# Performance work log

Measured on AMD Instinct MI355X. Metric: run time of the kernel, lower is better.

The kernel has to match this reference:

```python
import jax, jax.numpy as jnp
import numpy as np

B, N, CIN = 8, 4096, 64
S, K, C = 1024, 32, 128      # npoint, k, out_channels
J, DEPTH, H = 5, 2, 4
BETA, EPS = 0.05, 1e-5


def _fps(xyz, npoint):
    # farthest point sampling, deterministic start at index 0
    Bb, Nn = xyz.shape[0], xyz.shape[1]
    bidx = jnp.arange(Bb)

    def step(carry, _):
        dist, far = carry
        cen = xyz[bidx, far][:, None, :]              # [B,1,3]
        d = jnp.sum((xyz - cen) ** 2, -1)             # [B,N]
        dist = jnp.minimum(dist, d)
        nxt = jnp.argmax(dist, axis=1).astype(jnp.int32)
        return (dist, nxt), far

    init = (jnp.full((Bb, Nn), 1e10, xyz.dtype), jnp.zeros((Bb,), jnp.int32))
    _, idxs = jax.lax.scan(step, init, None, length=npoint)
    return idxs.T                                      # [B,npoint]


def _ln(x, g, b):
    mu = jnp.mean(x, -1, keepdims=True)
    v = jnp.mean((x - mu) ** 2, -1, keepdims=True)
    return (x - mu) * jax.lax.rsqrt(v + EPS) * g + b


def _forward(xyz, points, w1, g1, b1, w2, g2, b2, w3, g3, b3,
             ws, wb, alpha, wqkv, wo, ln1g, ln1b, ln2g, ln2b):
    gather = jax.vmap(lambda a, i: a[i])
    fps_idx = _fps(xyz, S)
    new_xyz = gather(xyz, fps_idx)                     # [B,S,3]
    # kNN: squared distances from centroids to all points
    d2 = (jnp.sum(new_xyz ** 2, -1)[:, :, None] + jnp.sum(xyz ** 2, -1)[:, None, :]
          - 2.0 * jnp.einsum('bsd,bnd->bsn', new_xyz, xyz))   # [B,S,N]
    idx = jax.lax.top_k(-d2, K)[1]                     # [B,S,K]
    flat = idx.reshape(B, S * K)
    gxyz = gather(xyz, flat).reshape(B, S, K, 3)
    gnorm = gxyz - new_xyz[:, :, None, :]              # relative coords
    gpts = gather(points, flat).reshape(B, S, K, CIN)
    h = jnp.concatenate([gnorm, gpts], -1)             # [B,S,K,67]
    # pointwise shared MLP (1x1 conv + BN(batch stats) + ReLU)
    for w, g, b in ((w1, g1, b1), (w2, g2, b2), (w3, g3, b3)):
        h = jnp.einsum('bskc,oc->bsko', h, w)
        m = jnp.mean(h, (0, 1, 2))
        v = jnp.var(h, (0, 1, 2))
        h = jax.nn.relu((h - m) * jax.lax.rsqrt(v + EPS) * g + b)
    P = B * S
    pf = h.reshape(P, K, C)
    px = gnorm.reshape(P, K, 3)
    # per-patch graph: Gaussian affinity, sigma = mean pairwise distance
    dd = jnp.sum((px[:, :, None] - px[:, None, :]) ** 2, -1)   # [P,K,K]
    sigma = jnp.mean(jnp.sqrt(dd + 1e-12), (1, 2))[:, None, None]
    A = jnp.exp(-dd / (2.0 * sigma ** 2 + 1e-12))
    dinv = jax.lax.rsqrt(jnp.sum(A, -1) + 1e-12)
    I = jnp.eye(K, dtype=pf.dtype)
    L = I - dinv[:, :, None] * A * dinv[:, None, :]
    # heat-kernel wavelets psi_j = exp(-s_j L), 4th-order Taylor
    psis = []
    for j in range(J):
        M = (-BETA * (2.0 ** j)) * L
        T = I + M
        acc = M
        for m in range(2, 5):
            acc = jnp.einsum('pkl,plm->pkm', acc, M) / m
            T = T + acc
        psis.append(T)
    hcur = pf
    for d in range(DEPTH):
        mix = jnp.zeros_like(hcur)
        for j in range(J):
            mix = mix + alpha[d, j] * jnp.einsum('pkl,plc,cd->pkd', psis[j], hcur, ws[d, j])
        hcur = _ln(hcur + jax.nn.relu(mix + wb[d]), ln1g[d], ln1b[d])
        qkv = (hcur @ wqkv[d]).reshape(P, K, 3, H, C // H)
        q, k_, v = qkv[:, :, 0], qkv[:, :, 1], qkv[:, :, 2]      # [P,K,H,dh]
        att = jax.nn.softmax(jnp.einsum('pkhd,plhd->phkl', q, k_) / np.sqrt(C // H).astype(np.float32), axis=-1)
        o = jnp.einsum('phkl,plhd->pkhd', att, v).reshape(P, K, C) @ wo[d]
        hcur = _ln(hcur + o, ln2g[d], ln2b[d])
    out = jnp.max(hcur.reshape(B, S, K, C), axis=2)    # max-pool over k
    return new_xyz, out


def setup_inputs() -> dict:
    key = jax.random.key(0)
    ks = jax.random.split(key, 10)
    nrm = lambda k, shp, sc: jax.random.normal(k, shp, jnp.float32) * sc
    cin = CIN + 3
    return {
        'xyz': jax.random.normal(ks[0], (B, N, 3), jnp.float32),
        'points': jax.random.normal(ks[1], (B, N, CIN), jnp.float32),
        'w1': nrm(ks[2], (64, cin), cin ** -0.5),
        'g1': jnp.ones((64,)), 'b1': jnp.zeros((64,)),
        'w2': nrm(ks[3], (64, 64), 64 ** -0.5),
        'g2': jnp.ones((64,)), 'b2': jnp.zeros((64,)),
        'w3': nrm(ks[4], (C, 64), 64 ** -0.5),
        'g3': jnp.ones((C,)), 'b3': jnp.zeros((C,)),
        'ws': nrm(ks[5], (DEPTH, J, C, C), C ** -0.5),
        'wb': jnp.zeros((DEPTH, C)),
        'alpha': jnp.ones((DEPTH, J)) / J,
        'wqkv': nrm(ks[6], (DEPTH, C, 3 * C), C ** -0.5),
        'wo': nrm(ks[7], (DEPTH, C, C), C ** -0.5),
        'ln1g': jnp.ones((DEPTH, C)), 'ln1b': jnp.zeros((DEPTH, C)),
        'ln2g': jnp.ones((DEPTH, C)), 'ln2b': jnp.zeros((DEPTH, C)),
    }


def reference(xyz, points, w1, g1, b1, w2, g2, b2, w3, g3, b3,
              ws, wb, alpha, wqkv, wo, ln1g, ln1b, ln2g, ln2b):
    return _forward(xyz, points, w1, g1, b1, w2, g2, b2, w3, g3, b3,
                    ws, wb, alpha, wqkv, wo, ln1g, ln1b, ln2g, ln2b)
```

## Files before the change

kernel.cpp:

```cpp
#include <hip/hip_runtime.h>
#include <math.h>

#define NB 8
#define NP 4096
#define NCIN 64
#define NS 1024
#define NK 32
#define NC 128
#define NJ 5
#define NDEPTH 2
#define NH 4
#define NPTS (NB*NS)
#define NM (NPTS*NK)
#define EPSF 1e-5f

typedef float f32x4 __attribute__((ext_vector_type(4)));
typedef short bf16x8 __attribute__((ext_vector_type(8)));
typedef unsigned short ushort_t;
typedef unsigned long long u64;

#define MFMA(a,b,c) __builtin_amdgcn_mfma_f32_16x16x32_bf16(a,b,c,0,0,0)

__device__ __forceinline__ ushort_t f2b(float f) {
  unsigned int u = __float_as_uint(f);
  u = (u + 0x7fffu + ((u >> 16) & 1u)) >> 16;
  return (ushort_t)u;
}
__device__ __forceinline__ float b2f(ushort_t h) {
  unsigned int u = ((unsigned int)h) << 16;
  return __uint_as_float(u);
}

template<int CTRL>
__device__ __forceinline__ float dpp_f(float v) {
  return __int_as_float(__builtin_amdgcn_update_dpp(0, __float_as_int(v), CTRL, 0xf, 0xf, true));
}
__device__ __forceinline__ float dpp_sum16(float v) {
  v += dpp_f<0xB1>(v); v += dpp_f<0x4E>(v);
  v += dpp_f<0x141>(v); v += dpp_f<0x140>(v);
  return v;
}
__device__ __forceinline__ float dpp_max16(float v) {
  v = fmaxf(v, dpp_f<0xB1>(v)); v = fmaxf(v, dpp_f<0x4E>(v));
  v = fmaxf(v, dpp_f<0x141>(v)); v = fmaxf(v, dpp_f<0x140>(v));
  return v;
}

#define DPPMAX(CTRL) { \
  unsigned lo2 = (unsigned)__builtin_amdgcn_update_dpp(0, (int)(unsigned)best, CTRL, 0xf, 0xf, true); \
  unsigned hi2 = (unsigned)__builtin_amdgcn_update_dpp(0, (int)(unsigned)(best >> 32), CTRL, 0xf, 0xf, true); \
  u64 o = ((u64)hi2 << 32) | lo2; \
  if (o > best) best = o; }

#define DPPMIN(CTRL) { \
  unsigned lo2 = (unsigned)__builtin_amdgcn_update_dpp((int)(unsigned)best, (int)(unsigned)best, CTRL, 0xf, 0xf, false); \
  unsigned hi2 = (unsigned)__builtin_amdgcn_update_dpp((int)(unsigned)(best >> 32), (int)(unsigned)(best >> 32), CTRL, 0xf, 0xf, false); \
  u64 o = ((u64)hi2 << 32) | lo2; \
  if (o < best) best = o; }

__global__ __launch_bounds__(256) void k_fps(const float* __restrict__ xyz,
                                             float* __restrict__ newxyz,
                                             const float* __restrict__ w1,
                                             ushort_t* __restrict__ wp1) {
  const int b = blockIdx.x;
  const int t = threadIdx.x;
  if (b >= NB) {
    int gid = (b - NB)*256 + t;
    int tile = gid >> 9, r = gid & 511;
    int tk = tile >> 2, tn = tile & 3;
    int lane2 = r >> 3, jj = r & 7;
    int k = tk*32 + (lane2 >> 4)*8 + jj;
    int n = tn*16 + (lane2 & 15);
    float v = (k < 67) ? w1[n*67 + k] : 0.0f;
    wp1[gid] = f2b(v);
    return;
  }
  const int lane = t & 63;
  const int w = t >> 6;
  __shared__ float Xl[NP*3];
  __shared__ float cenL[NS*3];
  __shared__ u64 slotP[2][4];
  __shared__ __align__(16) float slotC[2][4][4];
  const float* X = xyz + (size_t)b * NP * 3;
  for (int i = t; i < NP*3; i += 256) Xl[i] = X[i];
  __syncthreads();
  float px[16], py[16], pz[16], dist[16];
  unsigned inv[16];
#pragma unroll
  for (int i = 0; i < 16; ++i) {
    int n = t + 256*i;
    px[i] = Xl[3*n]; py[i] = Xl[3*n+1]; pz[i] = Xl[3*n+2];
    dist[i] = 1e10f;
    inv[i] = ~(unsigned)n;
  }
  float cx = Xl[0], cy = Xl[1], cz = Xl[2];
  for (int s = 0; s < NS; ++s) {
    if (t == 0) { cenL[3*s] = cx; cenL[3*s+1] = cy; cenL[3*s+2] = cz; }
    u64 best = 0;
#pragma unroll
    for (int i = 0; i < 16; ++i) {
      float dx = px[i]-cx, dy = py[i]-cy, dz = pz[i]-cz;
      float d = fmaf(dx,dx, fmaf(dy,dy, dz*dz));
      float nd = fminf(dist[i], d);
      dist[i] = nd;
      u64 p = ((u64)__float_as_uint(nd) << 32) | inv[i];
      best = p > best ? p : best;
    }
    DPPMAX(0x111)
    DPPMAX(0x112)
    DPPMAX(0x114)
    DPPMAX(0x118)
    DPPMAX(0x142)
    DPPMAX(0x143)
    if (lane == 63) {
      slotP[s&1][w] = best;
      int bi3 = 3 * (int)(~(unsigned)best);
      slotC[s&1][w][0] = Xl[bi3];
      slotC[s&1][w][1] = Xl[bi3+1];
      slotC[s&1][w][2] = Xl[bi3+2];
    }
    __syncthreads();
    const int par = s & 1;
    u64 s0 = slotP[par][0], s1 = slotP[par][1], s2 = slotP[par][2], s3 = slotP[par][3];
    f32x4 c0v = *(const f32x4*)&slotC[par][0][0];
    f32x4 c1v = *(const f32x4*)&slotC[par][1][0];
    f32x4 c2v = *(const f32x4*)&slotC[par][2][0];
    f32x4 c3v = *(const f32x4*)&slotC[par][3][0];
    u64 m = s0; f32x4 cw = c0v;
    if (s1 > m) { m = s1; cw = c1v; }
    if (s2 > m) { m = s2; cw = c2v; }
    if (s3 > m) { m = s3; cw = c3v; }
    cx = cw[0]; cy = cw[1]; cz = cw[2];
  }
  __syncthreads();
  float* o = newxyz + (size_t)b * NS * 3;
  for (int i = t; i < NS*3; i += 256) o[i] = cenL[i];
}

__global__ __launch_bounds__(64) void k_knn(const float* __restrict__ xyz,
                                            const float* __restrict__ newxyz,
                                            int* __restrict__ knn_idx,
                                            float* __restrict__ gnorm) {
  const int p = blockIdx.x;
  const int b = p >> 10;
  const int lane = threadIdx.x;
  const float* X = xyz + (size_t)b * NP * 3;
  __shared__ float d2[NP];
  float cx = newxyz[3*p], cy = newxyz[3*p+1], cz = newxyz[3*p+2];
  float sc = cx*cx + cy*cy + cz*cz;
#pragma unroll 4
  for (int i = 0; i < NP/64; ++i) {
    int n = lane + 64*i;
    float x = X[3*n], y = X[3*n+1], z = X[3*n+2];
    float sx = x*x + y*y + z*z;
    float dot = cx*x + cy*y + cz*z;
    d2[n] = sc + sx - 2.0f*dot;
  }
  for (int it = 0; it < NK; ++it) {
    float bv = 3.0e38f; int bi = 0x7fffffff;
#pragma unroll 8
    for (int i = 0; i < NP/64; ++i) {
      int n = lane + 64*i;
      float v = d2[n];
      if (v < bv) { bv = v; bi = n; }
    }
    unsigned ub = __float_as_uint(bv);
    ub ^= ((unsigned)((int)ub >> 31)) | 0x80000000u;
    u64 best = ((u64)ub << 32) | (unsigned)bi;
    DPPMIN(0x111)
    DPPMIN(0x112)
    DPPMIN(0x114)
    DPPMIN(0x118)
    DPPMIN(0x142)
    DPPMIN(0x143)
    u64 win = __shfl(best, 63);
    if (lane == 0) {
      int wi = (int)(unsigned)win;
      d2[wi] = 3.3e38f;
      knn_idx[p*NK + it] = wi;
      float* g = gnorm + ((size_t)p*NK + it)*3;
      g[0] = X[3*wi]   - cx;
      g[1] = X[3*wi+1] - cy;
      g[2] = X[3*wi+2] - cz;
    }
  }
}

__global__ __launch_bounds__(256) void k_layer1M(const float* __restrict__ points,
                                                 const int* __restrict__ knn_idx,
                                                 const float* __restrict__ gnorm,
                                                 const ushort_t* __restrict__ wp1,
                                                 float* __restrict__ y,
                                                 float* __restrict__ stats) {
  const int r0 = blockIdx.x * 64;
  const int t = threadIdx.x;
  const int lane = t & 63;
  const int w = t >> 6;
  const int lo16 = lane & 15;
  const int hi4 = lane >> 4;
  __shared__ __align__(16) ushort_t XbS[64*104];
  __shared__ int nid[64];
  __shared__ float ps[4][64], pss[4][64];
  if (t < 64) nid[t] = knn_idx[r0 + t];
  __syncthreads();
  for (int idx = t; idx < 64*67; idx += 256) {
    int r = idx / 67, c = idx % 67;
    int row = r0 + r;
    float v;
    if (c < 3) v = gnorm[(size_t)row*3 + c];
    else {
      int bb = row >> 15;
      int n = nid[r];
      v = points[((size_t)bb*NP + n)*NCIN + (c-3)];
    }
    XbS[r*104 + c] = f2b(v);
  }
  for (int idx = t; idx < 64*37; idx += 256) {
    int r = idx / 37, c = idx % 37;
    XbS[r*104 + 67 + c] = 0;
  }
  __syncthreads();
  const int arow = (w*16 + lo16)*104;
  float s1[4], s2[4];
#pragma unroll
  for (int tn = 0; tn < 4; ++tn) {
    f32x4 acc = {0.f,0.f,0.f,0.f};
#pragma unroll
    for (int tk = 0; tk < 3; ++tk) {
      bf16x8 a = *(const bf16x8*)(XbS + arow + tk*32 + hi4*8);
      bf16x8 b = *(const bf16x8*)(wp1 + ((tk*4 + tn) << 9) + (lane << 3));
      acc = MFMA(a, b, acc);
    }
    int col = tn*16 + lo16;
    int rbase = r0 + w*16 + hi4*4;
    float a1 = 0.f, a2 = 0.f;
#pragma unroll
    for (int r = 0; r < 4; ++r) {
      y[(size_t)(rbase + r)*64 + col] = acc[r];
      a1 += acc[r]; a2 += acc[r]*acc[r];
    }
    a1 += __shfl_xor(a1, 16); a1 += __shfl_xor(a1, 32);
    a2 += __shfl_xor(a2, 16); a2 += __shfl_xor(a2, 32);
    s1[tn] = a1; s2[tn] = a2;
  }
  if (hi4 == 0) {
#pragma unroll
    for (int tn = 0; tn < 4; ++tn) {
      ps[w][tn*16 + lo16]  = s1[tn];
      pss[w][tn*16 + lo16] = s2[tn];
    }
  }
  __syncthreads();
  if (t < 64) {
    atomicAdd(&stats[t],      ps[0][t]+ps[1][t]+ps[2][t]+ps[3][t]);
    atomicAdd(&stats[64 + t], pss[0][t]+pss[1][t]+pss[2][t]+pss[3][t]);
  }
}

template <int COUT>
__global__ __launch_bounds__(256) void k_layerM(const float* __restrict__ xin,
                                                const float* __restrict__ stats_in,
                                                const float* __restrict__ g,
                                                const float* __restrict__ bb_,
                                                const ushort_t* __restrict__ wp,
                                                float* __restrict__ y,
                                                float* __restrict__ stats) {
  const int r0 = blockIdx.x * 64;
  const int t = threadIdx.x;
  const int lane = t & 63;
  const int w = t >> 6;
  const int lo16 = lane & 15;
  const int hi4 = lane >> 4;
  constexpr int NTN = COUT >> 4;
  __shared__ __align__(16) ushort_t XbS[64*72];
  __shared__ float sa[64], sb[64];
  __shared__ float ps[4][COUT], pss[4][COUT];
  if (t < 64) {
    const float inv = 1.0f / (float)NM;
    float m = stats_in[t] * inv;
    float var = stats_in[64 + t] * inv - m*m;
    float a = g[t] * rsqrtf(var + EPSF);
    sa[t] = a;
    sb[t] = bb_[t] - m * a;
  }
  __syncthreads();
#pragma unroll
  for (int i = 0; i < 16; ++i) {
    int idx = t + 256*i;
    int r = idx >> 6, c = idx & 63;
    float v = xin[(size_t)r0*64 + idx];
    XbS[r*72 + c] = f2b(fmaxf(sa[c]*v + sb[c], 0.0f));
  }
  __syncthreads();
  const int arow = (w*16 + lo16)*72;
  float s1[NTN], s2[NTN];
#pragma unroll
  for (int tn = 0; tn < NTN; ++tn) {
    f32x4 acc = {0.f,0.f,0.f,0.f};
#pragma unroll
    for (int tk = 0; tk < 2; ++tk) {
      bf16x8 a = *(const bf16x8*)(XbS + arow + tk*32 + hi4*8);
      bf16x8 b = *(const bf16x8*)(wp + ((tk*NTN + tn) << 9) + (lane << 3));
      acc = MFMA(a, b, acc);
    }
    int col = tn*16 + lo16;
    int rbase = r0 + w*16 + hi4*4;
    float a1 = 0.f, a2 = 0.f;
#pragma unroll
    for (int r = 0; r < 4; ++r) {
      y[(size_t)(rbase + r)*COUT + col] = acc[r];
      a1 += acc[r]; a2 += acc[r]*acc[r];
    }
    a1 += __shfl_xor(a1, 16); a1 += __shfl_xor(a1, 32);
    a2 += __shfl_xor(a2, 16); a2 += __shfl_xor(a2, 32);
    s1[tn] = a1; s2[tn] = a2;
  }
  if (hi4 == 0) {
#pragma unroll
    for (int tn = 0; tn < NTN; ++tn) {
      ps[w][tn*16 + lo16]  = s1[tn];
      pss[w][tn*16 + lo16] = s2[tn];
    }
  }
  __syncthreads();
  if (t < COUT) {
    atomicAdd(&stats[t],        ps[0][t]+ps[1][t]+ps[2][t]+ps[3][t]);
    atomicAdd(&stats[COUT + t], pss[0][t]+pss[1][t]+pss[2][t]+pss[3][t]);
  }
}

__global__ __launch_bounds__(256) void k_pack(const float* __restrict__ ws,
                                              const float* __restrict__ wqkv,
                                              const float* __restrict__ wo,
                                              const float* __restrict__ w2,
                                              const float* __restrict__ w3,
                                              ushort_t* __restrict__ wpk) {
  int gid = blockIdx.x*256 + threadIdx.x;
  if (gid < 294912) {
    const float* src; int N_; int rem;
    if (gid < 163840)      { int mat = gid >> 14; rem = gid & 16383; src = ws  + (size_t)mat*16384; N_ = 128; }
    else if (gid < 262144) { int g2 = gid - 163840; int d = g2/49152; rem = g2 - d*49152; src = wqkv + (size_t)d*49152; N_ = 384; }
    else                   { int g3 = gid - 262144; int d = g3 >> 14; rem = g3 & 16383;  src = wo  + (size_t)d*16384; N_ = 128; }
    int NTN = N_ >> 4;
    int tile = rem >> 9, r = rem & 511;
    int tk = tile / NTN, tn = tile % NTN;
    int lane2 = r >> 3, jj = r & 7;
    int k = tk*32 + (lane2 >> 4)*8 + jj;
    int n = tn*16 + (lane2 & 15);
    wpk[gid] = f2b(src[(size_t)k*N_ + n]);
  } else if (gid < 299008) {
    int rem = gid - 294912;
    int tile = rem >> 9, r = rem & 511;
    int tk = tile >> 2, tn = tile & 3;
    int lane2 = r >> 3, jj = r & 7;
    int k = tk*32 + (lane2 >> 4)*8 + jj;
    int n = tn*16 + (lane2 & 15);
    wpk[gid] = f2b(w2[n*64 + k]);
  } else if (gid < 307200) {
    int rem = gid - 299008;
    int tile = rem >> 9, r = rem & 511;
    int tk = tile >> 3, tn = tile & 7;
    int lane2 = r >> 3, jj = r & 7;
    int k = tk*32 + (lane2 >> 4)*8 + jj;
    int n = tn*16 + (lane2 & 15);
    wpk[gid] = f2b(w3[n*64 + k]);
  }
}

__global__ __launch_bounds__(256, 2) void k_group(
    const float* __restrict__ h3,
    const float* __restrict__ stats3, const float* __restrict__ g3,
    const float* __restrict__ b3,
    const float* __restrict__ gnorm,
    const ushort_t* __restrict__ wpk,
    const float* __restrict__ wb, const float* __restrict__ alpha,
    const float* __restrict__ ln1g, const float* __restrict__ ln1b,
    const float* __restrict__ ln2g, const float* __restrict__ ln2b,
    float* __restrict__ out) {
  const int p = blockIdx.x;
  const int t = threadIdx.x;
  const int lane = t & 63;
  const int w = t >> 6;
  const int lo16 = lane & 15;
  const int hi4 = lane >> 4;

  __shared__ __align__(16) ushort_t hbS[NK*NC];
  __shared__ __align__(16) ushort_t psisS[5*32*40];
  __shared__ __align__(16) unsigned char scratch[27648];

  float*    ddAF = (float*)scratch;
  float*    pxF  = (float*)(scratch + 4224);
  float*    dinvF= (float*)(scratch + 4608);
  float*    sigF = (float*)(scratch + 4736);
  ushort_t* LbS  = (ushort_t*)(scratch + 4768);
  ushort_t* PmS  = (ushort_t*)(scratch + 7328);
  ushort_t* qS   = (ushort_t*)scratch;
  ushort_t* kS2  = (ushort_t*)(scratch + 8704);
  ushort_t* vTS  = (ushort_t*)(scratch + 17408);
  float*    rowStat = (float*)(scratch + 20480);
  float*    aff3S = rowStat;

  const int c0 = 32*w + lo16, c1 = c0 + 16;

  if (t < 128) {
    const float invn = 1.0f / (float)NM;
    float m = stats3[t] * invn;
    float var = stats3[128 + t] * invn - m*m;
    float a = g3[t] * rsqrtf(var + EPSF);
    aff3S[t] = a;
    aff3S[128 + t] = b3[t] - m * a;
  }
  if (t < 96) pxF[t] = gnorm[(size_t)p*96 + t];
  __syncthreads();
  const float* h3p = h3 + (size_t)p*4096;
#pragma unroll
  for (int i = 0; i < 16; ++i) {
    int idx = t + 256*i;
    int c = idx & 127, row = idx >> 7;
    float v = fmaxf(aff3S[c]*h3p[idx] + aff3S[128+c], 0.f);
    int ha = ((row << 8) + (c << 1)) ^ ((row & 7) << 4);
    hbS[ha >> 1] = f2b(v);
  }
  float hc[2][2][4];
  {
    float ga0 = aff3S[c0], gb0 = aff3S[128+c0];
    float ga1 = aff3S[c1], gb1 = aff3S[128+c1];
#pragma unroll
    for (int mi = 0; mi < 2; ++mi)
#pragma unroll
      for (int r = 0; r < 4; ++r) {
        int row = mi*16 + hi4*4 + r;
        hc[mi][0][r] = fmaxf(ga0*h3p[row*NC + c0] + gb0, 0.f);
        hc[mi][1][r] = fmaxf(ga1*h3p[row*NC + c1] + gb1, 0.f);
      }
  }
  __syncthreads();
  float part = 0.f;
  for (int i = t; i < 1024; i += 256) {
    int k = i >> 5, l = i & 31;
    float dx = pxF[k*3]  -pxF[l*3];
    float dy = pxF[k*3+1]-pxF[l*3+1];
    float dz = pxF[k*3+2]-pxF[l*3+2];
    float dd = dx*dx + dy*dy + dz*dz;
    ddAF[k*33+l] = dd;
    part += sqrtf(dd + 1e-12f);
  }
#pragma unroll
  for (int off = 32; off; off >>= 1) part += __shfl_xor(part, off);
  if (lane == 0) sigF[w] = part;
  __syncthreads();
  if (t == 0) {
    float sg = (sigF[0]+sigF[1]+sigF[2]+sigF[3]) * (1.0f/1024.0f);
    sigF[4] = 2.0f*sg*sg + 1e-12f;
  }
  __syncthreads();
  const float denom = sigF[4];
  for (int i = t; i < 1024; i += 256) {
    int k = i >> 5, l = i & 31;
    ddAF[k*33+l] = expf(-ddAF[k*33+l] / denom);
  }
  __syncthreads();
  {
    int row = t >> 3, e = t & 7;
    float s = ddAF[row*33 + e] + ddAF[row*33 + e + 8]
            + ddAF[row*33 + e + 16] + ddAF[row*33 + e + 24];
    s += __shfl_xor(s,1); s += __shfl_xor(s,2); s += __shfl_xor(s,4);
    if (e == 0) dinvF[row] = rsqrtf(s + 1e-12f);
  }
  __syncthreads();
  for (int i = t; i < 1024; i += 256) {
    int k = i >> 5, l = i & 31;
    float v = -(dinvF[k] * ddAF[k*33+l] * dinvF[l]);
    if (k == l) v += 1.0f;
    LbS[k*40+l] = f2b(v);
  }
  __syncthreads();
  {
    int mi2 = w >> 1, ni2 = w & 1;
    int arow = (mi2*16 + lo16)*80 + (hi4 << 4);
    int brow = (ni2*16 + lo16)*80 + (hi4 << 4);
    bf16x8 bfr = *(const bf16x8*)((const char*)LbS + brow);
#pragma unroll
    for (int m = 2; m <= 4; ++m) {
      const ushort_t* Asrc = (m == 2) ? LbS : (PmS + (m-3)*1280);
      bf16x8 afr = *(const bf16x8*)((const char*)Asrc + arow);
      f32x4 z = {0.f,0.f,0.f,0.f};
      f32x4 pv = MFMA(afr, bfr, z);
      int rb2 = mi2*16 + hi4*4;
      int cl = ni2*16 + lo16;
#pragma unroll
      for (int r = 0; r < 4; ++r) PmS[(m-2)*1280 + (rb2+r)*40 + cl] = f2b(pv[r]);
      __syncthreads();
    }
  }
  for (int i = t; i < 1024; i += 256) {
    int k = i >> 5, l = i & 31;
    float lb = b2f(LbS[k*40+l]);
    float p2 = b2f(PmS[k*40+l]);
    float p3 = b2f(PmS[1280 + k*40+l]);
    float p4 = b2f(PmS[2560 + k*40+l]);
    float diag = (k == l) ? 1.0f : 0.0f;
#pragma unroll
    for (int j = 0; j < NJ; ++j) {
      float sj = -0.05f * (float)(1 << j);
      float cc2 = 0.5f*sj*sj;
      float cc3 = cc2*sj*(1.0f/3.0f);
      float cc4 = cc3*sj*0.25f;
      psisS[j*1280 + k*40 + l] = f2b(diag + sj*lb + cc2*p2 + cc3*p3 + cc4*p4);
    }
  }

  for (int d = 0; d < NDEPTH; ++d) {
    f32x4 m00 = {0.f,0.f,0.f,0.f}, m01 = m00, m10 = m00, m11 = m00;
    for (int jp = 0; jp < 3; ++jp) {
      const int njp = (jp == 2) ? 1 : 2;
      __syncthreads();
      for (int jj = 0; jj < njp; ++jj) {
        int j = 2*jp + jj;
        ushort_t* HjS = (ushort_t*)scratch + jj*5120;
        const ushort_t* Wp = wpk + (size_t)(d*NJ + j)*16384;
        const float alj = alpha[d*NJ + j];
#pragma unroll
        for (int tni = 0; tni < 2; ++tni) {
          int tn = 2*w + tni;
          f32x4 acc0 = {0.f,0.f,0.f,0.f}, acc1 = acc0;
#pragma unroll
          for (int tk = 0; tk < 4; ++tk) {
            bf16x8 bfr = *(const bf16x8*)(Wp + ((tk*8 + tn) << 9) + (lane << 3));
            int row0 = lo16;
            int ba0 = ((row0 << 8) + (tk << 6) + (hi4 << 4)) ^ ((row0 & 7) << 4);
            bf16x8 a0 = *(const bf16x8*)((const char*)hbS + ba0);
            acc0 = MFMA(a0, bfr, acc0);
            int row1 = 16 + lo16;
            int ba1 = ((row1 << 8) + (tk << 6) + (hi4 << 4)) ^ ((row1 & 7) << 4);
            bf16x8 a1 = *(const bf16x8*)((const char*)hbS + ba1);
            acc1 = MFMA(a1, bfr, acc1);
          }
          int c = tn*16 + lo16;
          int rbase = hi4*4;
#pragma unroll
          for (int r = 0; r < 4; ++r) {
            HjS[c*40 + rbase + r]      = f2b(alj * acc0[r]);
            HjS[c*40 + 16 + rbase + r] = f2b(alj * acc1[r]);
          }
        }
      }
      __syncthreads();
      for (int jj = 0; jj < njp; ++jj) {
        int j = 2*jp + jj;
        const char* psj = (const char*)(psisS + j*1280);
        const char* HjB = (const char*)scratch + jj*10240;
        int koff = hi4 << 4;
        bf16x8 pa0 = *(const bf16x8*)(psj + lo16*80 + koff);
        bf16x8 pa1 = *(const bf16x8*)(psj + (16 + lo16)*80 + koff);
        bf16x8 hb0 = *(const bf16x8*)(HjB + c0*80 + koff);
        bf16x8 hb1 = *(const bf16x8*)(HjB + c1*80 + koff);
        m00 = MFMA(pa0, hb0, m00);
        m01 = MFMA(pa0, hb1, m01);
        m10 = MFMA(pa1, hb0, m10);
        m11 = MFMA(pa1, hb1, m11);
      }
    }
    float u[2][2][4];
    {
      float wb0 = wb[d*NC + c0], wb1 = wb[d*NC + c1];
#pragma unroll
      for (int r = 0; r < 4; ++r) {
        u[0][0][r] = hc[0][0][r] + fmaxf(m00[r] + wb0, 0.f);
        u[0][1][r] = hc[0][1][r] + fmaxf(m01[r] + wb1, 0.f);
        u[1][0][r] = hc[1][0][r] + fmaxf(m10[r] + wb0, 0.f);
        u[1][1][r] = hc[1][1][r] + fmaxf(m11[r] + wb1, 0.f);
      }
#pragma unroll
      for (int mi = 0; mi < 2; ++mi)
#pragma unroll
        for (int r = 0; r < 4; ++r) {
          float s = u[mi][0][r] + u[mi][1][r];
          float q = u[mi][0][r]*u[mi][0][r] + u[mi][1][r]*u[mi][1][r];
          s = dpp_sum16(s);
          q = dpp_sum16(q);
          if (lo16 == 0) {
            int row = mi*16 + hi4*4 + r;
            rowStat[row*8 + w*2]     = s;
            rowStat[row*8 + w*2 + 1] = q;
          }
        }
    }
    __syncthreads();
    {
      float g0 = ln1g[d*NC + c0], b0 = ln1b[d*NC + c0];
      float g1 = ln1g[d*NC + c1], b1 = ln1b[d*NC + c1];
#pragma unroll
      for (int mi = 0; mi < 2; ++mi)
#pragma unroll
        for (int r = 0; r < 4; ++r) {
          int row = mi*16 + hi4*4 + r;
          f32x4 a = *(const f32x4*)(rowStat + row*8);
          f32x4 bq = *(const f32x4*)(rowStat + row*8 + 4);
          float mu = (a[0]+a[2]+bq[0]+bq[2]) * (1.0f/128.0f);
          float ex2 = (a[1]+a[3]+bq[1]+bq[3]) * (1.0f/128.0f);
          float rs = rsqrtf(ex2 - mu*mu + EPSF);
          float h0 = (u[mi][0][r] - mu)*rs*g0 + b0;
          float h1 = (u[mi][1][r] - mu)*rs*g1 + b1;
          hc[mi][0][r] = h0; hc[mi][1][r] = h1;
          int ha0 = ((row << 8) + (c0 << 1)) ^ ((row & 7) << 4);
          int ha1 = ((row << 8) + (c1 << 1)) ^ ((row & 7) << 4);
          hbS[ha0 >> 1] = f2b(h0);
          hbS[ha1 >> 1] = f2b(h1);
        }
    }
    __syncthreads();
    const ushort_t* Wq = wpk + 163840 + (size_t)d*49152;
#pragma unroll
    for (int ti = 0; ti < 12; ++ti) {
      int tile = w + 4*ti;
      int mi = (tile >= 24) ? 1 : 0;
      int tn = tile - 24*mi;
      int comp = tn >> 3;
      int cb = (tn & 7) * 16;
      f32x4 acc = {0.f,0.f,0.f,0.f};
#pragma unroll
      for (int tk = 0; tk < 4; ++tk) {
        bf16x8 bfr = *(const bf16x8*)(Wq + ((tk*24 + tn) << 9) + (lane << 3));
        int row = mi*16 + lo16;
        int ba = ((row << 8) + (tk << 6) + (hi4 << 4)) ^ ((row & 7) << 4);
        bf16x8 a = *(const bf16x8*)((const char*)hbS + ba);
        acc = MFMA(a, bfr, acc);
      }
      int cl = cb + lo16;
      int rb2 = mi*16 + hi4*4;
      if (comp == 0) {
#pragma unroll
        for (int r = 0; r < 4; ++r) qS[(rb2+r)*136 + cl] = f2b(acc[r]);
      } else if (comp == 1) {
#pragma unroll
        for (int r = 0; r < 4; ++r) kS2[(rb2+r)*136 + cl] = f2b(acc[r]);
      } else {
#pragma unroll
        for (int r = 0; r < 4; ++r) vTS[cl*40 + rb2 + r] = f2b(acc[r]);
      }
    }
    __syncthreads();
    float scr[2][2][4];
#pragma unroll
    for (int ti = 0; ti < 2; ++ti) {
      int pi = w + 4*ti;
      int h = pi >> 1, mi = pi & 1;
      int koff = h*64 + (hi4 << 4);
      bf16x8 qa = *(const bf16x8*)((const char*)qS + (mi*16 + lo16)*272 + koff);
#pragma unroll
      for (int ni = 0; ni < 2; ++ni) {
        bf16x8 kb = *(const bf16x8*)((const char*)kS2 + (ni*16 + lo16)*272 + koff);
        f32x4 z = {0.f,0.f,0.f,0.f};
        f32x4 sv = MFMA(qa, kb, z);
#pragma unroll
        for (int r = 0; r < 4; ++r) scr[ti][ni][r] = sv[r] * 0.17677669529663687f;
      }
    }
    __syncthreads();
#pragma unroll
    for (int ti = 0; ti < 2; ++ti) {
      int pi = w + 4*ti;
      int h = pi >> 1, mi = pi & 1;
#pragma unroll
      for (int r = 0; r < 4; ++r) {
        float s0 = scr[ti][0][r], s1 = scr[ti][1][r];
        float mx = dpp_max16(fmaxf(s0, s1));
        float e0 = expf(s0 - mx), e1 = expf(s1 - mx);
        float sum = dpp_sum16(e0 + e1);
        float iv = 1.0f / sum;
        int row = mi*16 + hi4*4 + r;
        qS[row*136 + h*32 + lo16]      = f2b(e0*iv);
        qS[row*136 + h*32 + 16 + lo16] = f2b(e1*iv);
      }
    }
    __syncthreads();
#pragma unroll
    for (int ti = 0; ti < 4; ++ti) {
      int tile = w + 4*ti;
      int h = tile >> 2, mi = (tile >> 1) & 1, ni = tile & 1;
      bf16x8 aa = *(const bf16x8*)((const char*)qS + (mi*16 + lo16)*272 + h*64 + (hi4 << 4));
      bf16x8 vb = *(const bf16x8*)((const char*)vTS + (h*32 + ni*16 + lo16)*80 + (hi4 << 4));
      f32x4 z = {0.f,0.f,0.f,0.f};
      f32x4 ov = MFMA(aa, vb, z);
      int col = h*32 + ni*16 + lo16;
      int rb2 = mi*16 + hi4*4;
#pragma unroll
      for (int r = 0; r < 4; ++r) {
        int row = rb2 + r;
        int ha = ((row << 8) + (col << 1)) ^ ((row & 7) << 4);
        hbS[ha >> 1] = f2b(ov[r]);
      }
    }
    __syncthreads();
    const ushort_t* Wop = wpk + 262144 + (size_t)d*16384;
#pragma unroll
    for (int tni = 0; tni < 2; ++tni) {
      int tn = 2*w + tni;
      f32x4 acc0 = {0.f,0.f,0.f,0.f}, acc1 = acc0;
#pragma unroll
      for (int tk = 0; tk < 4; ++tk) {
        bf16x8 bfr = *(const bf16x8*)(Wop + ((tk*8 + tn) << 9) + (lane << 3));
        int row0 = lo16;
        int ba0 = ((row0 << 8) + (tk << 6) + (hi4 << 4)) ^ ((row0 & 7) << 4);
        bf16x8 a0 = *(const bf16x8*)((const char*)hbS + ba0);
        acc0 = MFMA(a0, bfr, acc0);
        int row1 = 16 + lo16;
        int ba1 = ((row1 << 8) + (tk << 6) + (hi4 << 4)) ^ ((row1 & 7) << 4);
        bf16x8 a1 = *(const bf16x8*)((const char*)hbS + ba1);
        acc1 = MFMA(a1, bfr, acc1);
      }
#pragma unroll
      for (int r = 0; r < 4; ++r) {
        u[0][tni][r] = hc[0][tni][r] + acc0[r];
        u[1][tni][r] = hc[1][tni][r] + acc1[r];
      }
    }
#pragma unroll
    for (int mi = 0; mi < 2; ++mi)
#pragma unroll
      for (int r = 0; r < 4; ++r) {
        float s = u[mi][0][r] + u[mi][1][r];
        float q = u[mi][0][r]*u[mi][0][r] + u[mi][1][r]*u[mi][1][r];
        s = dpp_sum16(s);
        q = dpp_sum16(q);
        if (lo16 == 0) {
          int row = mi*16 + hi4*4 + r;
          rowStat[row*8 + w*2]     = s;
          rowStat[row*8 + w*2 + 1] = q;
        }
      }
    __syncthreads();
    {
      float g0 = ln2g[d*NC + c0], b0 = ln2b[d*NC + c0];
      float g1 = ln2g[d*NC + c1], b1 = ln2b[d*NC + c1];
#pragma unroll
      for (int mi = 0; mi < 2; ++mi)
#pragma unroll
        for (int r = 0; r < 4; ++r) {
          int row = mi*16 + hi4*4 + r;
          f32x4 a = *(const f32x4*)(rowStat + row*8);
          f32x4 bq = *(const f32x4*)(rowStat + row*8 + 4);
          float mu = (a[0]+a[2]+bq[0]+bq[2]) * (1.0f/128.0f);
          float ex2 = (a[1]+a[3]+bq[1]+bq[3]) * (1.0f/128.0f);
          float rs = rsqrtf(ex2 - mu*mu + EPSF);
          float h0 = (u[mi][0][r] - mu)*rs*g0 + b0;
          float h1 = (u[mi][1][r] - mu)*rs*g1 + b1;
          hc[mi][0][r] = h0; hc[mi][1][r] = h1;
          int ha0 = ((row << 8) + (c0 << 1)) ^ ((row & 7) << 4);
          int ha1 = ((row << 8) + (c1 << 1)) ^ ((row & 7) << 4);
          hbS[ha0 >> 1] = f2b(h0);
          hbS[ha1 >> 1] = f2b(h1);
        }
    }
  }
  {
    float v0 = hc[0][0][0], v1 = hc[0][1][0];
#pragma unroll
    for (int r = 1; r < 4; ++r) { v0 = fmaxf(v0, hc[0][0][r]); v1 = fmaxf(v1, hc[0][1][r]); }
#pragma unroll
    for (int r = 0; r < 4; ++r) { v0 = fmaxf(v0, hc[1][0][r]); v1 = fmaxf(v1, hc[1][1][r]); }
    v0 = fmaxf(v0, __shfl_xor(v0, 16)); v0 = fmaxf(v0, __shfl_xor(v0, 32));
    v1 = fmaxf(v1, __shfl_xor(v1, 16)); v1 = fmaxf(v1, __shfl_xor(v1, 32));
    if (hi4 == 0) {
      out[(size_t)p*NC + c0] = v0;
      out[(size_t)p*NC + c1] = v1;
    }
  }
}

extern "C" void kernel_launch(void* const* d_in, const int* in_sizes, int n_in,
                              void* d_out, int out_size, void* d_ws, size_t ws_size,
                              hipStream_t stream) {
  const float* xyz    = (const float*)d_in[0];
  const float* points = (const float*)d_in[1];
  const float* w1     = (const float*)d_in[2];
  const float* g1     = (const float*)d_in[3];
  const float* b1     = (const float*)d_in[4];
  const float* w2     = (const float*)d_in[5];
  const float* g2     = (const float*)d_in[6];
  const float* b2     = (const float*)d_in[7];
  const float* w3     = (const float*)d_in[8];
  const float* g3     = (const float*)d_in[9];
  const float* b3     = (const float*)d_in[10];
  const float* wsW    = (const float*)d_in[11];
  const float* wb     = (const float*)d_in[12];
  const float* alpha  = (const float*)d_in[13];
  const float* wqkv   = (const float*)d_in[14];
  const float* wo     = (const float*)d_in[15];
  const float* ln1g   = (const float*)d_in[16];
  const float* ln1b   = (const float*)d_in[17];
  const float* ln2g   = (const float*)d_in[18];
  const float* ln2b   = (const float*)d_in[19];
  float* outp = (float*)d_out;

  float* wsf   = (float*)d_ws;
  float* gnorm = wsf;
  float* stats = wsf + 786432;
  int*   knn   = (int*)(wsf + 787968);
  ushort_t* wpk = (ushort_t*)(wsf + 787968);
  float* h2    = wsf + 1050112;
  float* hX    = wsf + 17827328;
  ushort_t* wp1 = (ushort_t*)(wsf + 17827328 + 16777216);

  hipMemsetAsync(stats, 0, 768*sizeof(float), stream);
  k_fps<<<NB + 24, 256, 0, stream>>>(xyz, outp, w1, wp1);
  k_knn<<<NPTS, 64, 0, stream>>>(xyz, outp, knn, gnorm);
  k_layer1M<<<NM/64, 256, 0, stream>>>(points, knn, gnorm, wp1, hX, stats);
  k_pack<<<307200/256, 256, 0, stream>>>(wsW, wqkv, wo, w2, w3, wpk);
  k_layerM<64><<<NM/64, 256, 0, stream>>>(hX, stats, g1, b1, wpk + 294912, h2, stats + 256);
  k_layerM<128><<<NM/64, 256, 0, stream>>>(h2, stats + 256, g2, b2, wpk + 299008, hX, stats + 512);
  k_group<<<NPTS, 256, 0, stream>>>(hX, stats + 512, g3, b3, gnorm, wpk, wb, alpha,
                                    ln1g, ln1b, ln2g, ln2b, outp + (size_t)NB*NS*3);
}
```

Before: 1.699 ms.

## Fold weight packing into FPS launch, split FPS argmax chain, add MFMA priority hints

Weight packing moves out of its own launch and runs as extra blocks of the FPS kernel, where it fills idle CUs during the serial FPS phase. To make room, the kNN index buffer is moved into the h2 region so it no longer aliases the packed weights. The FPS per-thread max reduction is split into two independent chains for more ILP on the serial critical path. s_setprio hints are added around the MFMA sections of k_group so matrix-issuing waves get scheduling priority.

New measurement: 1.721 ms. Within noise of the previous version (+1.3%).

```diff
diff --git a/kernel.cpp b/kernel.cpp
--- a/kernel.cpp
+++ b/kernel.cpp
@@ -61,9 +61,48 @@
 __global__ __launch_bounds__(256) void k_fps(const float* __restrict__ xyz,
                                              float* __restrict__ newxyz,
                                              const float* __restrict__ w1,
-                                             ushort_t* __restrict__ wp1) {
+                                             ushort_t* __restrict__ wp1,
+                                             const float* __restrict__ ws,
+                                             const float* __restrict__ wqkv,
+                                             const float* __restrict__ wo,
+                                             const float* __restrict__ w2,
+                                             const float* __restrict__ w3,
+                                             ushort_t* __restrict__ wpk) {
   const int b = blockIdx.x;
   const int t = threadIdx.x;
+  if (b >= NB + 24) {
+    int gid = (b - NB - 24)*256 + t;
+    if (gid < 294912) {
+      const float* src; int N_; int rem;
+      if (gid < 163840)      { int mat = gid >> 14; rem = gid & 16383; src = ws  + (size_t)mat*16384; N_ = 128; }
+      else if (gid < 262144) { int g2 = gid - 163840; int d = g2/49152; rem = g2 - d*49152; src = wqkv + (size_t)d*49152; N_ = 384; }
+      else                   { int g3 = gid - 262144; int d = g3 >> 14; rem = g3 & 16383;  src = wo  + (size_t)d*16384; N_ = 128; }
+      int NTN = N_ >> 4;
+      int tile = rem >> 9, r = rem & 511;
+      int tk = tile / NTN, tn = tile % NTN;
+      int lane2 = r >> 3, jj = r & 7;
+      int k = tk*32 + (lane2 >> 4)*8 + jj;
+      int n = tn*16 + (lane2 & 15);
+      wpk[gid] = f2b(src[(size_t)k*N_ + n]);
+    } else if (gid < 299008) {
+      int rem = gid - 294912;
+      int tile = rem >> 9, r = rem & 511;
+      int tk = tile >> 2, tn = tile & 3;
+      int lane2 = r >> 3, jj = r & 7;
+      int k = tk*32 + (lane2 >> 4)*8 + jj;
+      int n = tn*16 + (lane2 & 15);
+      wpk[gid] = f2b(w2[n*64 + k]);
+    } else if (gid < 307200) {
+      int rem = gid - 299008;
+      int tile = rem >> 9, r = rem & 511;
+      int tk = tile >> 3, tn = tile & 7;
+      int lane2 = r >> 3, jj = r & 7;
+      int k = tk*32 + (lane2 >> 4)*8 + jj;
+      int n = tn*16 + (lane2 & 15);
+      wpk[gid] = f2b(w3[n*64 + k]);
+    }
+    return;
+  }
   if (b >= NB) {
     int gid = (b - NB)*256 + t;
     int tile = gid >> 9, r = gid & 511;
@@ -96,16 +135,23 @@
   float cx = Xl[0], cy = Xl[1], cz = Xl[2];
   for (int s = 0; s < NS; ++s) {
     if (t == 0) { cenL[3*s] = cx; cenL[3*s+1] = cy; cenL[3*s+2] = cz; }
-    u64 best = 0;
-#pragma unroll
-    for (int i = 0; i < 16; ++i) {
-      float dx = px[i]-cx, dy = py[i]-cy, dz = pz[i]-cz;
-      float d = fmaf(dx,dx, fmaf(dy,dy, dz*dz));
-      float nd = fminf(dist[i], d);
-      dist[i] = nd;
-      u64 p = ((u64)__float_as_uint(nd) << 32) | inv[i];
-      best = p > best ? p : best;
-    }
+    u64 b0 = 0, b1 = 0;
+#pragma unroll
+    for (int i = 0; i < 16; i += 2) {
+      float dx0 = px[i]-cx, dy0 = py[i]-cy, dz0 = pz[i]-cz;
+      float d0 = fmaf(dx0,dx0, fmaf(dy0,dy0, dz0*dz0));
+      float nd0 = fminf(dist[i], d0);
+      dist[i] = nd0;
+      u64 p0 = ((u64)__float_as_uint(nd0) << 32) | inv[i];
+      b0 = p0 > b0 ? p0 : b0;
+      float dx1 = px[i+1]-cx, dy1 = py[i+1]-cy, dz1 = pz[i+1]-cz;
+      float d1 = fmaf(dx1,dx1, fmaf(dy1,dy1, dz1*dz1));
+      float nd1 = fminf(dist[i+1], d1);
+      dist[i+1] = nd1;
+      u64 p1 = ((u64)__float_as_uint(nd1) << 32) | inv[i+1];
+      b1 = p1 > b1 ? p1 : b1;
+    }
+    u64 best = b1 > b0 ? b1 : b0;
     DPPMAX(0x111)
     DPPMAX(0x112)
     DPPMAX(0x114)
@@ -329,44 +375,6 @@
   }
 }
 
-__global__ __launch_bounds__(256) void k_pack(const float* __restrict__ ws,
-                                              const float* __restrict__ wqkv,
-                                              const float* __restrict__ wo,
-                                              const float* __restrict__ w2,
-                                              const float* __restrict__ w3,
-                                              ushort_t* __restrict__ wpk) {
-  int gid = blockIdx.x*256 + threadIdx.x;
-  if (gid < 294912) {
-    const float* src; int N_; int rem;
-    if (gid < 163840)      { int mat = gid >> 14; rem = gid & 16383; src = ws  + (size_t)mat*16384; N_ = 128; }
-    else if (gid < 262144) { int g2 = gid - 163840; int d = g2/49152; rem = g2 - d*49152; src = wqkv + (size_t)d*49152; N_ = 384; }
-    else                   { int g3 = gid - 262144; int d = g3 >> 14; rem = g3 & 16383;  src = wo  + (size_t)d*16384; N_ = 128; }
-    int NTN = N_ >> 4;
-    int tile = rem >> 9, r = rem & 511;
-    int tk = tile / NTN, tn = tile % NTN;
-    int lane2 = r >> 3, jj = r & 7;
-    int k = tk*32 + (lane2 >> 4)*8 + jj;
-    int n = tn*16 + (lane2 & 15);
-    wpk[gid] = f2b(src[(size_t)k*N_ + n]);
-  } else if (gid < 299008) {
-    int rem = gid - 294912;
-    int tile = rem >> 9, r = rem & 511;
-    int tk = tile >> 2, tn = tile & 3;
-    int lane2 = r >> 3, jj = r & 7;
-    int k = tk*32 + (lane2 >> 4)*8 + jj;
-    int n = tn*16 + (lane2 & 15);
-    wpk[gid] = f2b(w2[n*64 + k]);
-  } else if (gid < 307200) {
-    int rem = gid - 299008;
-    int tile = rem >> 9, r = rem & 511;
-    int tk = tile >> 3, tn = tile & 7;
-    int lane2 = r >> 3, jj = r & 7;
-    int k = tk*32 + (lane2 >> 4)*8 + jj;
-    int n = tn*16 + (lane2 & 15);
-    wpk[gid] = f2b(w3[n*64 + k]);
-  }
-}
-
 __global__ __launch_bounds__(256, 2) void k_group(
     const float* __restrict__ h3,
     const float* __restrict__ stats3, const float* __restrict__ g3,
@@ -520,6 +528,7 @@
         ushort_t* HjS = (ushort_t*)scratch + jj*5120;
         const ushort_t* Wp = wpk + (size_t)(d*NJ + j)*16384;
         const float alj = alpha[d*NJ + j];
+        __builtin_amdgcn_s_setprio(1);
 #pragma unroll
         for (int tni = 0; tni < 2; ++tni) {
           int tn = 2*w + tni;
@@ -544,8 +553,10 @@
             HjS[c*40 + 16 + rbase + r] = f2b(alj * acc1[r]);
           }
         }
+        __builtin_amdgcn_s_setprio(0);
       }
       __syncthreads();
+      __builtin_amdgcn_s_setprio(1);
       for (int jj = 0; jj < njp; ++jj) {
         int j = 2*jp + jj;
         const char* psj = (const char*)(psisS + j*1280);
@@ -560,6 +571,7 @@
         m10 = MFMA(pa1, hb0, m10);
         m11 = MFMA(pa1, hb1, m11);
       }
+      __builtin_amdgcn_s_setprio(0);
     }
     float u[2][2][4];
     {
@@ -611,6 +623,7 @@
     }
     __syncthreads();
     const ushort_t* Wq = wpk + 163840 + (size_t)d*49152;
+    __builtin_amdgcn_s_setprio(1);
 #pragma unroll
     for (int ti = 0; ti < 12; ++ti) {
       int tile = w + 4*ti;
@@ -640,6 +653,7 @@
         for (int r = 0; r < 4; ++r) vTS[cl*40 + rb2 + r] = f2b(acc[r]);
       }
     }
+    __builtin_amdgcn_s_setprio(0);
     __syncthreads();
     float scr[2][2][4];
 #pragma unroll
@@ -694,6 +708,7 @@
     }
     __syncthreads();
     const ushort_t* Wop = wpk + 262144 + (size_t)d*16384;
+    __builtin_amdgcn_s_setprio(1);
 #pragma unroll
     for (int tni = 0; tni < 2; ++tni) {
       int tn = 2*w + tni;
@@ -716,6 +731,7 @@
         u[1][tni][r] = hc[1][tni][r] + acc1[r];
       }
     }
+    __builtin_amdgcn_s_setprio(0);
 #pragma unroll
     for (int mi = 0; mi < 2; ++mi)
 #pragma unroll
@@ -797,17 +813,17 @@
   float* wsf   = (float*)d_ws;
   float* gnorm = wsf;
   float* stats = wsf + 786432;
-  int*   knn   = (int*)(wsf + 787968);
   ushort_t* wpk = (ushort_t*)(wsf + 787968);
   float* h2    = wsf + 1050112;
+  int*   knn   = (int*)h2;
   float* hX    = wsf + 17827328;
   ushort_t* wp1 = (ushort_t*)(wsf + 17827328 + 16777216);
 
   hipMemsetAsync(stats, 0, 768*sizeof(float), stream);
-  k_fps<<<NB + 24, 256, 0, stream>>>(xyz, outp, w1, wp1);
+  k_fps<<<NB + 24 + 1200, 256, 0, stream>>>(xyz, outp, w1, wp1,
+                                            wsW, wqkv, wo, w2, w3, wpk);
   k_knn<<<NPTS, 64, 0, stream>>>(xyz, outp, knn, gnorm);
   k_layer1M<<<NM/64, 256, 0, stream>>>(points, knn, gnorm, wp1, hX, stats);
-  k_pack<<<307200/256, 256, 0, stream>>>(wsW, wqkv, wo, w2, w3, wpk);
   k_layerM<64><<<NM/64, 256, 0, stream>>>(hX, stats, g1, b1, wpk + 294912, h2, stats + 256);
   k_layerM<128><<<NM/64, 256, 0, stream>>>(h2, stats + 256, g2, b2, wpk + 299008, hX, stats + 512);
   k_group<<<NPTS, 256, 0, stream>>>(hX, stats + 512, g3, b3, gnorm, wpk, wb, alpha,
```
